# Performance work log

Hardware: AMD Instinct MI355X
Metric: run time of the kernel (lower is better)

Reference implementation:

```python
import jax, jax.numpy as jnp
import numpy as np

BETA, ALPHA, NS_STEPS = 0.9, 1.0, 1
D_MODEL, D_STATE, D_CONV, EXPAND = 768, 16, 4, 2
D_INNER = EXPAND * D_MODEL
DT_RANK = -(-D_MODEL // 16)  # ceil(d_model/16) = 48
B, L = 2, 1024


def setup_inputs() -> dict:
    key = jax.random.key(0)
    ks = jax.random.split(key, 8)
    s = lambda k, shape, sc=0.02: jax.random.normal(k, shape, jnp.float32) * sc
    return {
        "hidden_states": jax.random.normal(ks[0], (B, L, D_MODEL), jnp.float32),
        "in_proj_w": s(ks[1], (2 * D_INNER, D_MODEL)),
        "conv_w": s(ks[2], (D_INNER, 1, D_CONV), 0.2),
        "conv_b": jnp.zeros((D_INNER,), jnp.float32),
        "x_proj_w": s(ks[3], (DT_RANK + 2 * D_STATE, D_INNER)),
        "dt_head_w": s(ks[4], (D_INNER, DT_RANK)),
        "dt_head_b": s(ks[5], (D_INNER,), 0.1),
        "out_proj_w": s(ks[6], (D_MODEL, D_INNER)),
        "D": jnp.ones((D_INNER,), jnp.float32),
    }


def _newton_schulz(G, steps):
    """Muon-style quintic Newton-Schulz orthogonalization of (b, d, n) with d >= n."""
    a, b, c = 3.4445, -4.7750, 2.0315
    X = G / (jnp.linalg.norm(G, axis=(-2, -1), keepdims=True) + 1e-7)
    X = X.swapaxes(-2, -1)  # (b, n, d): rows <= cols
    for _ in range(steps):
        A = X @ X.swapaxes(-2, -1)       # (b, n, n) small Gram
        Bm = b * A + c * (A @ A)
        X = a * X + Bm @ X
    return X.swapaxes(-2, -1)            # back to (b, d, n)


def reference(hidden_states, in_proj_w, conv_w, conv_b, x_proj_w, dt_head_w, dt_head_b, out_proj_w, D):
    Bz, Lz, _ = hidden_states.shape
    dtype = hidden_states.dtype
    # input projection -> x, z  (B, L, d_inner) each
    xz = jnp.einsum('bld,ed->ble', hidden_states, in_proj_w)
    x, z = jnp.split(xz, 2, axis=-1)
    # causal depthwise conv over time + SiLU
    xc = jax.lax.conv_general_dilated(
        x.swapaxes(1, 2), conv_w, (1,), [(D_CONV - 1, 0)],
        dimension_numbers=('NCH', 'OIH', 'NCH'), feature_group_count=D_INNER)
    x = jax.nn.silu(xc.swapaxes(1, 2) + conv_b)  # (B, L, d_inner)
    # projections for dt / k / q
    x_dbl = jnp.einsum('bld,ed->ble', x, x_proj_w)
    dt_low, k, q = jnp.split(x_dbl, [DT_RANK, DT_RANK + D_STATE], axis=-1)
    dt = jnp.einsum('blr,dr->bld', dt_low, dt_head_w)  # (B, L, d_inner), bias applied in scan

    def step(carry, inp):
        v, h = carry  # velocity / hidden states, each (b, d_inner, d_state)
        x_t, dt_t, k_t, q_t = inp
        dt_t = jax.nn.sigmoid(dt_t + dt_head_b)                              # (b, d)
        dt_t = dt_t / (1.0 + dt_t * jnp.sum(k_t * k_t, axis=-1, keepdims=True))
        dA = 1.0 - dt_t[:, :, None] * (k_t * k_t)[:, None, :]                # (b, d, n)
        G = (dt_t * x_t)[:, :, None] * k_t[:, None, :]                       # dt * u * k
        v = BETA * v + ALPHA * _newton_schulz(G, NS_STEPS)
        h = dA * h + v
        y_t = jnp.einsum('bdn,bn->bd', h, q_t) + D * x_t
        return (v, h), y_t

    init = (jnp.zeros((Bz, D_INNER, D_STATE), dtype),
            jnp.zeros((Bz, D_INNER, D_STATE), dtype))
    xs = (x.swapaxes(0, 1), dt.swapaxes(0, 1), k.swapaxes(0, 1), q.swapaxes(0, 1))
    _, y = jax.lax.scan(step, init, xs)        # (L, B, d_inner)
    y = y.swapaxes(0, 1) * jax.nn.silu(z)      # gate
    return jnp.einsum('bld,od->blo', y, out_proj_w)
```

## Files before the change

### kernel.cpp

```cpp
#include <hip/hip_runtime.h>

#define D_MODEL 768
#define D_STATE 16
#define D_INNER 1536
#define DT_RANK 48
#define NB 2
#define LSEQ 1024
#define NROWS (NB * LSEQ)
#define CCH 8
#define CLEN (LSEQ / CCH)
#define BETA_CL 1.3900845e-06f

typedef __attribute__((ext_vector_type(4))) float f32x4;
typedef __attribute__((ext_vector_type(8))) short s16x8;
typedef __attribute__((ext_vector_type(8))) unsigned short u16x8;

__device__ __forceinline__ unsigned short f2bu(float f) {
  unsigned int x = __builtin_bit_cast(unsigned int, f);
  x += 0x7fffu + ((x >> 16) & 1u);
  return (unsigned short)(x >> 16);
}

template <bool ATOMIC>
__global__ __launch_bounds__(256) void gemm_bt(const float* __restrict__ A,
                                               const float* __restrict__ B,
                                               float* __restrict__ C, int M, int N, int K,
                                               int lda, int ldb, int ldc, int kseg_len) {
  __shared__ __align__(16) unsigned short As[2][64][40];
  __shared__ __align__(16) unsigned short Bs[2][64][40];
  const int m0 = blockIdx.y * 64, n0 = blockIdx.x * 64;
  const int kbeg = blockIdx.z * kseg_len;
  const int kend = (kbeg + kseg_len < K) ? (kbeg + kseg_len) : K;
  const int t = threadIdx.x;
  const int wave = t >> 6, lane = t & 63;
  const int wm = wave >> 1, wn = wave & 1;
  const int quad = lane >> 4, l16 = lane & 15;
  const int srow = t >> 2;
  const int kseg = (t & 3) * 8;
  const float* Ap = A + (size_t)(m0 + srow) * lda;
  const float* Bp = B + (size_t)(n0 + srow) * ldb;
  const bool va = (m0 + srow) < M, vb = (n0 + srow) < N;

  f32x4 ra0, ra1, rb0, rb1;
  auto pref = [&](int k0) {
    const int kk = k0 + kseg;
    const int krem = kend - kk;
    if (va && krem >= 8) {
      ra0 = *(const f32x4*)(Ap + kk);
      ra1 = *(const f32x4*)(Ap + kk + 4);
    } else {
#pragma unroll
      for (int j = 0; j < 4; j++) {
        ra0[j] = (va && j < krem) ? Ap[kk + j] : 0.0f;
        ra1[j] = (va && j + 4 < krem) ? Ap[kk + j + 4] : 0.0f;
      }
    }
    if (vb && krem >= 8) {
      rb0 = *(const f32x4*)(Bp + kk);
      rb1 = *(const f32x4*)(Bp + kk + 4);
    } else {
#pragma unroll
      for (int j = 0; j < 4; j++) {
        rb0[j] = (vb && j < krem) ? Bp[kk + j] : 0.0f;
        rb1[j] = (vb && j + 4 < krem) ? Bp[kk + j + 4] : 0.0f;
      }
    }
  };
  auto tolds = [&](int bi) {
    u16x8 oa, ob;
#pragma unroll
    for (int j = 0; j < 4; j++) {
      oa[j] = f2bu(ra0[j]); oa[4 + j] = f2bu(ra1[j]);
      ob[j] = f2bu(rb0[j]); ob[4 + j] = f2bu(rb1[j]);
    }
    *(u16x8*)&As[bi][srow][kseg] = oa;
    *(u16x8*)&Bs[bi][srow][kseg] = ob;
  };

  f32x4 acc[2][2] = {};
  pref(kbeg);
  tolds(0);
  __syncthreads();
  int buf = 0;
  for (int k0 = kbeg; k0 < kend; k0 += 32) {
    const bool more = (k0 + 32 < kend);
    if (more) pref(k0 + 32);
    s16x8 a0 = *(const s16x8*)&As[buf][wm * 32 + l16][quad * 8];
    s16x8 a1 = *(const s16x8*)&As[buf][wm * 32 + 16 + l16][quad * 8];
    s16x8 b0 = *(const s16x8*)&Bs[buf][wn * 32 + l16][quad * 8];
    s16x8 b1 = *(const s16x8*)&Bs[buf][wn * 32 + 16 + l16][quad * 8];
    acc[0][0] = __builtin_amdgcn_mfma_f32_16x16x32_bf16(a0, b0, acc[0][0], 0, 0, 0);
    acc[0][1] = __builtin_amdgcn_mfma_f32_16x16x32_bf16(a0, b1, acc[0][1], 0, 0, 0);
    acc[1][0] = __builtin_amdgcn_mfma_f32_16x16x32_bf16(a1, b0, acc[1][0], 0, 0, 0);
    acc[1][1] = __builtin_amdgcn_mfma_f32_16x16x32_bf16(a1, b1, acc[1][1], 0, 0, 0);
    if (more) tolds(buf ^ 1);
    __syncthreads();
    buf ^= 1;
  }
#pragma unroll
  for (int mi = 0; mi < 2; mi++)
#pragma unroll
    for (int ni = 0; ni < 2; ni++)
#pragma unroll
      for (int r = 0; r < 4; r++) {
        int row = m0 + wm * 32 + mi * 16 + quad * 4 + r;
        int col = n0 + wn * 32 + ni * 16 + l16;
        if (row < M && col < N) {
          if constexpr (ATOMIC)
            atomicAdd(&C[(size_t)row * ldc + col], acc[mi][ni][r]);
          else
            C[(size_t)row * ldc + col] = acc[mi][ni][r];
        }
      }
}

__global__ __launch_bounds__(256) void conv_silu_kernel(const float* __restrict__ xz,
                                                        const float* __restrict__ cw,
                                                        const float* __restrict__ cb,
                                                        float* __restrict__ xc) {
  int idx = blockIdx.x * 256 + threadIdx.x;
  if (idx >= NROWS * D_INNER) return;
  int c = idx % D_INNER;
  int row = idx / D_INNER;
  int l = row & (LSEQ - 1);
  float acc = cb[c];
#pragma unroll
  for (int j = 0; j < 4; j++) {
    int dl = l - 3 + j;
    if (dl >= 0) acc += xz[(size_t)(row - 3 + j) * 3072 + c] * cw[c * 4 + j];
  }
  float sg = 1.0f / (1.0f + expf(-acc));
  xc[idx] = acc * sg;
}

__global__ __launch_bounds__(256) void precompute_kernel(const float* __restrict__ xdbl,
                                                         float* __restrict__ dtbuf,
                                                         const float* __restrict__ xconv,
                                                         const float* __restrict__ dtb,
                                                         float* __restrict__ ubuf,
                                                         float* __restrict__ kqbuf) {
  int row = blockIdx.x;
  int t = threadIdx.x;
  const float* xr = xdbl + (size_t)row * 80;
  float nk = 0.0f;
#pragma unroll
  for (int n = 0; n < 16; n++) { float kv = xr[48 + n]; nk += kv * kv; }
  float dtf[6], u0[6];
  float nupart = 0.0f;
#pragma unroll
  for (int i = 0; i < 6; i++) {
    int d = i * 256 + t;
    float draw = dtbuf[(size_t)row * D_INNER + d] + dtb[d];
    float sg = 1.0f / (1.0f + expf(-draw));
    float dv = sg / (1.0f + sg * nk);
    dtf[i] = dv;
    float u = dv * xconv[(size_t)row * D_INNER + d];
    u0[i] = u;
    nupart += u * u;
  }
  __shared__ float red[4];
  float v = nupart;
#pragma unroll
  for (int off = 32; off > 0; off >>= 1) v += __shfl_xor(v, off);
  if ((t & 63) == 0) red[t >> 6] = v;
  __syncthreads();
  float nu = red[0] + red[1] + red[2] + red[3];
  float p = nu * nk;
  float s = sqrtf(p) + 1e-7f;
  float tt = p / (s * s);
  float gamma = (3.4445f + tt * (-4.7750f + 2.0315f * tt)) / s;
#pragma unroll
  for (int i = 0; i < 6; i++) {
    int d = i * 256 + t;
    dtbuf[(size_t)row * D_INNER + d] = dtf[i];
    ubuf[(size_t)row * D_INNER + d] = gamma * u0[i];
  }
  if (t < 16) {
    kqbuf[(size_t)row * 32 + t] = xr[48 + t];
    kqbuf[(size_t)row * 32 + 16 + t] = xr[64 + t];
  }
}

__global__ __launch_bounds__(64) void scan_phase1(const float* __restrict__ ubuf,
                                                  const float* __restrict__ dtbuf,
                                                  const float* __restrict__ kqbuf,
                                                  float* __restrict__ cvp,
                                                  float* __restrict__ chp,
                                                  float* __restrict__ gp,
                                                  float* __restrict__ rp) {
  __shared__ float u_s[2][32][16];
  __shared__ float dt_s[2][32][16];
  __shared__ __align__(16) float kq_s[2][32][32];
  const int t = threadIdx.x;
  const int nq = t & 3, dloc = t >> 2;
  const int b = blockIdx.x / (96 * CCH);
  const int rem = blockIdx.x % (96 * CCH);
  const int d0 = (rem / CCH) * 16;
  const int c = rem % CCH;
  const int tbase = c * CLEN;
  const size_t ub = (size_t)b * LSEQ * D_INNER + d0;
  const float* kqb = kqbuf + (size_t)b * LSEQ * 32;
  const int scol = t & 15, srow0 = t >> 4;
  const int krow0 = t >> 3, kcol = (t & 7) * 4;
  float pu[8], pd[8];
  f32x4 pk[4];
  auto prefetch = [&](int t0) {
#pragma unroll
    for (int i = 0; i < 8; i++) {
      size_t off = ub + (size_t)(t0 + srow0 + 4 * i) * D_INNER + scol;
      pu[i] = ubuf[off];
      pd[i] = dtbuf[off];
    }
#pragma unroll
    for (int i = 0; i < 4; i++)
      pk[i] = *(const f32x4*)(kqb + (size_t)(t0 + krow0 + 8 * i) * 32 + kcol);
  };
  auto writelds = [&](int bi) {
#pragma unroll
    for (int i = 0; i < 8; i++) {
      u_s[bi][srow0 + 4 * i][scol] = pu[i];
      dt_s[bi][srow0 + 4 * i][scol] = pd[i];
    }
#pragma unroll
    for (int i = 0; i < 4; i++)
      *(f32x4*)&kq_s[bi][krow0 + 8 * i][kcol] = pk[i];
  };
  f32x4 v = {0.f, 0.f, 0.f, 0.f}, h = {0.f, 0.f, 0.f, 0.f};
  f32x4 g = {0.f, 0.f, 0.f, 0.f}, r = {1.f, 1.f, 1.f, 1.f};
  float bt = 0.9f;
  prefetch(tbase);
  writelds(0);
  int buf = 0;
  for (int t0 = 0; t0 < CLEN; t0 += 32) {
    const bool more = (t0 + 32 < CLEN);
    if (more) prefetch(tbase + t0 + 32);
#pragma unroll 4
    for (int s = 0; s < 32; s++) {
      float u = u_s[buf][s][dloc];
      float dtf = dt_s[buf][s][dloc];
      f32x4 kv = *(const f32x4*)&kq_s[buf][s][nq * 4];
#pragma unroll
      for (int j = 0; j < 4; j++) {
        float kj = kv[j];
        v[j] = fmaf(0.9f, v[j], u * kj);
        float a = fmaf(-dtf * kj, kj, 1.0f);
        h[j] = fmaf(a, h[j], v[j]);
        r[j] *= a;
        g[j] = fmaf(a, g[j], bt);
      }
      bt *= 0.9f;
    }
    if (more) writelds(buf ^ 1);
    buf ^= 1;
  }
  size_t o = (((size_t)b * CCH + c) * D_INNER + d0 + dloc) * 16 + nq * 4;
  *(f32x4*)(cvp + o) = v;
  *(f32x4*)(chp + o) = h;
  *(f32x4*)(gp + o) = g;
  *(f32x4*)(rp + o) = r;
}

__global__ __launch_bounds__(256) void scan_phase2(const float* __restrict__ cvp,
                                                   const float* __restrict__ chp,
                                                   float* __restrict__ gp,
                                                   float* __restrict__ rp) {
  int i = blockIdx.x * 256 + threadIdx.x;
  int b = i / (D_INNER * 16);
  int rem = i % (D_INNER * 16);
  float v0 = 0.f, h0 = 0.f;
#pragma unroll
  for (int c = 0; c < CCH; c++) {
    size_t o = ((size_t)(b * CCH + c)) * (D_INNER * 16) + rem;
    float cv = cvp[o], ch = chp[o], gg = gp[o], rr = rp[o];
    gp[o] = v0;
    rp[o] = h0;
    float v0n = fmaf(BETA_CL, v0, cv);
    float h0n = fmaf(gg, v0, fmaf(rr, h0, ch));
    v0 = v0n;
    h0 = h0n;
  }
}

__global__ __launch_bounds__(64) void scan_phase3(const float* __restrict__ ubuf,
                                                  const float* __restrict__ dtbuf,
                                                  const float* __restrict__ kqbuf,
                                                  const float* __restrict__ gp,
                                                  const float* __restrict__ rp,
                                                  float* __restrict__ ybuf) {
  __shared__ float u_s[2][32][16];
  __shared__ float dt_s[2][32][16];
  __shared__ __align__(16) float kq_s[2][32][32];
  const int t = threadIdx.x;
  const int nq = t & 3, dloc = t >> 2;
  const int b = blockIdx.x / (96 * CCH);
  const int rem = blockIdx.x % (96 * CCH);
  const int d0 = (rem / CCH) * 16;
  const int c = rem % CCH;
  const int tbase = c * CLEN;
  const size_t ub = (size_t)b * LSEQ * D_INNER + d0;
  const float* kqb = kqbuf + (size_t)b * LSEQ * 32;
  float* y_p = ybuf + (size_t)b * LSEQ * D_INNER + d0 + dloc;
  const int scol = t & 15, srow0 = t >> 4;
  const int krow0 = t >> 3, kcol = (t & 7) * 4;
  float pu[8], pd[8];
  f32x4 pk[4];
  auto prefetch = [&](int t0) {
#pragma unroll
    for (int i = 0; i < 8; i++) {
      size_t off = ub + (size_t)(t0 + srow0 + 4 * i) * D_INNER + scol;
      pu[i] = ubuf[off];
      pd[i] = dtbuf[off];
    }
#pragma unroll
    for (int i = 0; i < 4; i++)
      pk[i] = *(const f32x4*)(kqb + (size_t)(t0 + krow0 + 8 * i) * 32 + kcol);
  };
  auto writelds = [&](int bi) {
#pragma unroll
    for (int i = 0; i < 8; i++) {
      u_s[bi][srow0 + 4 * i][scol] = pu[i];
      dt_s[bi][srow0 + 4 * i][scol] = pd[i];
    }
#pragma unroll
    for (int i = 0; i < 4; i++)
      *(f32x4*)&kq_s[bi][krow0 + 8 * i][kcol] = pk[i];
  };
  size_t so = (((size_t)b * CCH + c) * D_INNER + d0 + dloc) * 16 + nq * 4;
  f32x4 v = *(const f32x4*)(gp + so);
  f32x4 h = *(const f32x4*)(rp + so);
  prefetch(tbase);
  writelds(0);
  int buf = 0;
  for (int t0 = 0; t0 < CLEN; t0 += 32) {
    const bool more = (t0 + 32 < CLEN);
    if (more) prefetch(tbase + t0 + 32);
#pragma unroll 4
    for (int s = 0; s < 32; s++) {
      float u = u_s[buf][s][dloc];
      float dtf = dt_s[buf][s][dloc];
      f32x4 kv = *(const f32x4*)&kq_s[buf][s][nq * 4];
      f32x4 qv = *(const f32x4*)&kq_s[buf][s][16 + nq * 4];
      float yp = 0.0f;
#pragma unroll
      for (int j = 0; j < 4; j++) {
        float kj = kv[j];
        v[j] = fmaf(0.9f, v[j], u * kj);
        float dA = fmaf(-dtf * kj, kj, 1.0f);
        h[j] = fmaf(dA, h[j], v[j]);
        yp = fmaf(h[j], qv[j], yp);
      }
      yp += __shfl_xor(yp, 1);
      yp += __shfl_xor(yp, 2);
      if (nq == 0) y_p[(size_t)(tbase + t0 + s) * D_INNER] = yp;
    }
    if (more) writelds(buf ^ 1);
    buf ^= 1;
  }
}

__global__ __launch_bounds__(256) void gate_kernel(const float* __restrict__ ybuf,
                                                   const float* __restrict__ xconv,
                                                   const float* __restrict__ xz,
                                                   const float* __restrict__ Dp,
                                                   float* __restrict__ yg) {
  int idx = blockIdx.x * 256 + threadIdx.x;
  if (idx >= NROWS * D_INNER) return;
  int c = idx % D_INNER;
  int row = idx / D_INNER;
  float z = xz[(size_t)row * 3072 + 1536 + c];
  float sz = z / (1.0f + expf(-z));
  yg[idx] = (ybuf[idx] + Dp[c] * xconv[idx]) * sz;
}

extern "C" void kernel_launch(void* const* d_in, const int* in_sizes, int n_in,
                              void* d_out, int out_size, void* d_ws, size_t ws_size,
                              hipStream_t stream) {
  const float* hidden = (const float*)d_in[0];
  const float* w_in   = (const float*)d_in[1];
  const float* conv_w = (const float*)d_in[2];
  const float* conv_b = (const float*)d_in[3];
  const float* w_x    = (const float*)d_in[4];
  const float* w_dt   = (const float*)d_in[5];
  const float* b_dt   = (const float*)d_in[6];
  const float* w_out  = (const float*)d_in[7];
  const float* Dp     = (const float*)d_in[8];

  float* ws    = (float*)d_ws;
  float* xz    = ws;
  float* xconv = xz + (size_t)NROWS * 3072;
  float* xdbl  = xconv + (size_t)NROWS * D_INNER;
  float* dtbuf = xdbl + (size_t)NROWS * 80;
  float* ubuf  = dtbuf + (size_t)NROWS * D_INNER;
  float* kqbuf = ubuf + (size_t)NROWS * D_INNER;
  float* ybuf  = kqbuf + (size_t)NROWS * 32;
  const size_t PL = (size_t)NB * CCH * D_INNER * 16;
  float* cvp   = ybuf + (size_t)NROWS * D_INNER;
  float* chp   = cvp + PL;
  float* gp    = chp + PL;
  float* rp    = gp + PL;
  float* yg    = ubuf;

  dim3 blk(256);
  hipMemsetAsync(xdbl, 0, (size_t)NROWS * 80 * 4, stream);
  hipMemsetAsync(d_out, 0, (size_t)NROWS * 768 * 4, stream);

  gemm_bt<false><<<dim3(48, 32, 1), blk, 0, stream>>>(hidden, w_in, xz, 2048, 3072, 768,
                                                      768, 768, 3072, 768);
  conv_silu_kernel<<<dim3(12288), blk, 0, stream>>>(xz, conv_w, conv_b, xconv);
  gemm_bt<true><<<dim3(2, 32, 8), blk, 0, stream>>>(xconv, w_x, xdbl, 2048, 80, 1536,
                                                    1536, 1536, 80, 192);
  gemm_bt<false><<<dim3(24, 32, 1), blk, 0, stream>>>(xdbl, w_dt, dtbuf, 2048, 1536, 48,
                                                      80, 48, 1536, 48);
  precompute_kernel<<<dim3(NROWS), blk, 0, stream>>>(xdbl, dtbuf, xconv, b_dt, ubuf, kqbuf);
  scan_phase1<<<dim3(NB * 96 * CCH), dim3(64), 0, stream>>>(ubuf, dtbuf, kqbuf, cvp, chp, gp, rp);
  scan_phase2<<<dim3(192), blk, 0, stream>>>(cvp, chp, gp, rp);
  scan_phase3<<<dim3(NB * 96 * CCH), dim3(64), 0, stream>>>(ubuf, dtbuf, kqbuf, gp, rp, ybuf);
  gate_kernel<<<dim3(12288), blk, 0, stream>>>(ybuf, xconv, xz, Dp, yg);
  gemm_bt<true><<<dim3(12, 32, 2), blk, 0, stream>>>(yg, w_out, (float*)d_out, 2048, 768, 1536,
                                                     1536, 1536, 768, 768);
}
```

Measured before the change: 242.1 us.

## Pre-convert GEMM operands to bf16 in producer kernels and a batched cast

Adds a single cast kernel that converts the hidden states and all four weight matrices to bf16 on every call. The conv and gate kernels now also emit bf16 copies of their outputs, so most GEMMs load 16-bit operands directly instead of loading fp32 and rounding inside each tile. This halves the operand bytes the GEMMs read and drops the conversion from their inner loop. In exchange it adds one launch and extra write traffic, and the output projection's split-K count goes from 2 to 4, which means more atomic adds.

```diff
diff --git a/kernel.cpp b/kernel.cpp
--- a/kernel.cpp
+++ b/kernel.cpp
@@ -21,9 +21,39 @@
   return (unsigned short)(x >> 16);
 }
 
-template <bool ATOMIC>
-__global__ __launch_bounds__(256) void gemm_bt(const float* __restrict__ A,
-                                               const float* __restrict__ B,
+#define CVT_TOTAL 663552
+__global__ __launch_bounds__(256) void cvt5_kernel(const float* __restrict__ s0,
+                                                   const float* __restrict__ s1,
+                                                   const float* __restrict__ s2,
+                                                   const float* __restrict__ s3,
+                                                   const float* __restrict__ s4,
+                                                   unsigned short* __restrict__ d0,
+                                                   unsigned short* __restrict__ d1,
+                                                   unsigned short* __restrict__ d2,
+                                                   unsigned short* __restrict__ d3,
+                                                   unsigned short* __restrict__ d4) {
+  int g = blockIdx.x * 256 + threadIdx.x;
+  if (g >= CVT_TOTAL) return;
+  const float* s;
+  unsigned short* d;
+  int base;
+  if (g < 196608)      { s = s0; d = d0; base = 0; }
+  else if (g < 491520) { s = s1; d = d1; base = 196608; }
+  else if (g < 506880) { s = s2; d = d2; base = 491520; }
+  else if (g < 516096) { s = s3; d = d3; base = 506880; }
+  else                 { s = s4; d = d4; base = 516096; }
+  int i = (g - base) * 8;
+  f32x4 a = *(const f32x4*)(s + i);
+  f32x4 b = *(const f32x4*)(s + i + 4);
+  u16x8 o;
+#pragma unroll
+  for (int j = 0; j < 4; j++) { o[j] = f2bu(a[j]); o[4 + j] = f2bu(b[j]); }
+  *(u16x8*)(d + i) = o;
+}
+
+template <bool AF32, bool ATOMIC>
+__global__ __launch_bounds__(256) void gemm_bt(const void* __restrict__ Av,
+                                               const unsigned short* __restrict__ B,
                                                float* __restrict__ C, int M, int N, int K,
                                                int lda, int ldb, int ldc, int kseg_len) {
   __shared__ __align__(16) unsigned short As[2][64][40];
@@ -37,44 +67,55 @@
   const int quad = lane >> 4, l16 = lane & 15;
   const int srow = t >> 2;
   const int kseg = (t & 3) * 8;
-  const float* Ap = A + (size_t)(m0 + srow) * lda;
-  const float* Bp = B + (size_t)(n0 + srow) * ldb;
   const bool va = (m0 + srow) < M, vb = (n0 + srow) < N;
-
-  f32x4 ra0, ra1, rb0, rb1;
+  const float* Af = (const float*)Av;
+  const unsigned short* Ab = (const unsigned short*)Av;
+  const unsigned short* Bp = B + (size_t)(n0 + srow) * ldb;
+
+  f32x4 ra0, ra1;
+  u16x8 rab;
+  u16x8 rbb;
   auto pref = [&](int k0) {
     const int kk = k0 + kseg;
     const int krem = kend - kk;
-    if (va && krem >= 8) {
-      ra0 = *(const f32x4*)(Ap + kk);
-      ra1 = *(const f32x4*)(Ap + kk + 4);
+    if constexpr (AF32) {
+      const float* Ap = Af + (size_t)(m0 + srow) * lda + kk;
+      if (va && krem >= 8) {
+        ra0 = *(const f32x4*)Ap;
+        ra1 = *(const f32x4*)(Ap + 4);
+      } else {
+#pragma unroll
+        for (int j = 0; j < 4; j++) {
+          ra0[j] = (va && j < krem) ? Ap[j] : 0.0f;
+          ra1[j] = (va && j + 4 < krem) ? Ap[j + 4] : 0.0f;
+        }
+      }
     } else {
-#pragma unroll
-      for (int j = 0; j < 4; j++) {
-        ra0[j] = (va && j < krem) ? Ap[kk + j] : 0.0f;
-        ra1[j] = (va && j + 4 < krem) ? Ap[kk + j + 4] : 0.0f;
+      const unsigned short* Ap = Ab + (size_t)(m0 + srow) * lda + kk;
+      if (va && krem >= 8) {
+        rab = *(const u16x8*)Ap;
+      } else {
+#pragma unroll
+        for (int j = 0; j < 8; j++) rab[j] = (va && j < krem) ? Ap[j] : (unsigned short)0;
       }
     }
     if (vb && krem >= 8) {
-      rb0 = *(const f32x4*)(Bp + kk);
-      rb1 = *(const f32x4*)(Bp + kk + 4);
+      rbb = *(const u16x8*)(Bp + kk);
     } else {
 #pragma unroll
-      for (int j = 0; j < 4; j++) {
-        rb0[j] = (vb && j < krem) ? Bp[kk + j] : 0.0f;
-        rb1[j] = (vb && j + 4 < krem) ? Bp[kk + j + 4] : 0.0f;
-      }
+      for (int j = 0; j < 8; j++) rbb[j] = (vb && j < krem) ? Bp[kk + j] : (unsigned short)0;
     }
   };
   auto tolds = [&](int bi) {
-    u16x8 oa, ob;
-#pragma unroll
-    for (int j = 0; j < 4; j++) {
-      oa[j] = f2bu(ra0[j]); oa[4 + j] = f2bu(ra1[j]);
-      ob[j] = f2bu(rb0[j]); ob[4 + j] = f2bu(rb1[j]);
-    }
-    *(u16x8*)&As[bi][srow][kseg] = oa;
-    *(u16x8*)&Bs[bi][srow][kseg] = ob;
+    if constexpr (AF32) {
+      u16x8 oa;
+#pragma unroll
+      for (int j = 0; j < 4; j++) { oa[j] = f2bu(ra0[j]); oa[4 + j] = f2bu(ra1[j]); }
+      *(u16x8*)&As[bi][srow][kseg] = oa;
+    } else {
+      *(u16x8*)&As[bi][srow][kseg] = rab;
+    }
+    *(u16x8*)&Bs[bi][srow][kseg] = rbb;
   };
 
   f32x4 acc[2][2] = {};
@@ -117,7 +158,8 @@
 __global__ __launch_bounds__(256) void conv_silu_kernel(const float* __restrict__ xz,
                                                         const float* __restrict__ cw,
                                                         const float* __restrict__ cb,
-                                                        float* __restrict__ xc) {
+                                                        float* __restrict__ xc,
+                                                        unsigned short* __restrict__ xcb) {
   int idx = blockIdx.x * 256 + threadIdx.x;
   if (idx >= NROWS * D_INNER) return;
   int c = idx % D_INNER;
@@ -130,7 +172,9 @@
     if (dl >= 0) acc += xz[(size_t)(row - 3 + j) * 3072 + c] * cw[c * 4 + j];
   }
   float sg = 1.0f / (1.0f + expf(-acc));
-  xc[idx] = acc * sg;
+  float val = acc * sg;
+  xc[idx] = val;
+  xcb[idx] = f2bu(val);
 }
 
 __global__ __launch_bounds__(256) void precompute_kernel(const float* __restrict__ xdbl,
@@ -362,14 +406,14 @@
                                                    const float* __restrict__ xconv,
                                                    const float* __restrict__ xz,
                                                    const float* __restrict__ Dp,
-                                                   float* __restrict__ yg) {
+                                                   unsigned short* __restrict__ ygb) {
   int idx = blockIdx.x * 256 + threadIdx.x;
   if (idx >= NROWS * D_INNER) return;
   int c = idx % D_INNER;
   int row = idx / D_INNER;
   float z = xz[(size_t)row * 3072 + 1536 + c];
   float sz = z / (1.0f + expf(-z));
-  yg[idx] = (ybuf[idx] + Dp[c] * xconv[idx]) * sz;
+  ygb[idx] = f2bu((ybuf[idx] + Dp[c] * xconv[idx]) * sz);
 }
 
 extern "C" void kernel_launch(void* const* d_in, const int* in_sizes, int n_in,
@@ -398,24 +442,33 @@
   float* chp   = cvp + PL;
   float* gp    = chp + PL;
   float* rp    = gp + PL;
-  float* yg    = ubuf;
+  unsigned short* bfr = (unsigned short*)(rp + PL);
+  unsigned short* hbf = bfr;
+  unsigned short* wib = hbf + 1572864;
+  unsigned short* wxb = wib + 2359296;
+  unsigned short* wdb = wxb + 122880;
+  unsigned short* wob = wdb + 73728;
+  unsigned short* xcb = wob + 1179648;
+  unsigned short* ygb = xcb + 3145728;
 
   dim3 blk(256);
   hipMemsetAsync(xdbl, 0, (size_t)NROWS * 80 * 4, stream);
   hipMemsetAsync(d_out, 0, (size_t)NROWS * 768 * 4, stream);
 
-  gemm_bt<false><<<dim3(48, 32, 1), blk, 0, stream>>>(hidden, w_in, xz, 2048, 3072, 768,
-                                                      768, 768, 3072, 768);
-  conv_silu_kernel<<<dim3(12288), blk, 0, stream>>>(xz, conv_w, conv_b, xconv);
-  gemm_bt<true><<<dim3(2, 32, 8), blk, 0, stream>>>(xconv, w_x, xdbl, 2048, 80, 1536,
-                                                    1536, 1536, 80, 192);
-  gemm_bt<false><<<dim3(24, 32, 1), blk, 0, stream>>>(xdbl, w_dt, dtbuf, 2048, 1536, 48,
-                                                      80, 48, 1536, 48);
+  cvt5_kernel<<<dim3(CVT_TOTAL / 256), blk, 0, stream>>>(hidden, w_in, w_x, w_dt, w_out,
+                                                         hbf, wib, wxb, wdb, wob);
+  gemm_bt<false, false><<<dim3(48, 32, 1), blk, 0, stream>>>(hbf, wib, xz, 2048, 3072, 768,
+                                                             768, 768, 3072, 768);
+  conv_silu_kernel<<<dim3(12288), blk, 0, stream>>>(xz, conv_w, conv_b, xconv, xcb);
+  gemm_bt<false, true><<<dim3(2, 32, 8), blk, 0, stream>>>(xcb, wxb, xdbl, 2048, 80, 1536,
+                                                           1536, 1536, 80, 192);
+  gemm_bt<true, false><<<dim3(24, 32, 1), blk, 0, stream>>>(xdbl, wdb, dtbuf, 2048, 1536, 48,
+                                                            80, 48, 1536, 48);
   precompute_kernel<<<dim3(NROWS), blk, 0, stream>>>(xdbl, dtbuf, xconv, b_dt, ubuf, kqbuf);
   scan_phase1<<<dim3(NB * 96 * CCH), dim3(64), 0, stream>>>(ubuf, dtbuf, kqbuf, cvp, chp, gp, rp);
   scan_phase2<<<dim3(192), blk, 0, stream>>>(cvp, chp, gp, rp);
   scan_phase3<<<dim3(NB * 96 * CCH), dim3(64), 0, stream>>>(ubuf, dtbuf, kqbuf, gp, rp, ybuf);
-  gate_kernel<<<dim3(12288), blk, 0, stream>>>(ybuf, xconv, xz, Dp, yg);
-  gemm_bt<true><<<dim3(12, 32, 2), blk, 0, stream>>>(yg, w_out, (float*)d_out, 2048, 768, 1536,
-                                                     1536, 1536, 768, 768);
-}
+  gate_kernel<<<dim3(12288), blk, 0, stream>>>(ybuf, xconv, xz, Dp, ygb);
+  gemm_bt<false, true><<<dim3(12, 32, 4), blk, 0, stream>>>(ygb, wob, (float*)d_out, 2048, 768,
+                                                            1536, 1536, 1536, 768, 384);
+}
```

Measured after the change: 239.8 us. No clear change (-1.0%).
